# Kernel optimization log

Measured on AMD Instinct MI355X. Metric: run time of the kernel, lower is better.

Reference implementation:

```python
import jax, jax.numpy as jnp
import numpy as np
from jax import lax

B, T, D, H, L = 64, 512, 768, 256, 9


def _lstm_dir(x, Wih, Whh, b, reverse):
    # x: [B,T,in]; Wih: [4H,in]; Whh: [4H,H]; b: [4H] (b_ih + b_hh fused).
    # PyTorch LSTM gate order: i, f, g, o.
    Hh = Whh.shape[1]
    xg = jnp.einsum('bti,gi->btg', x, Wih) + b  # precompute input contribution [B,T,4H]

    def step(carry, xt):
        h, c = carry
        g = xt + h @ Whh.T
        i, f, gg, o = jnp.split(g, 4, axis=-1)
        c = jax.nn.sigmoid(f) * c + jax.nn.sigmoid(i) * jnp.tanh(gg)
        h = jax.nn.sigmoid(o) * jnp.tanh(c)
        return (h, c), h

    h0 = jnp.zeros((x.shape[0], Hh), x.dtype)
    _, hs = lax.scan(step, (h0, h0), jnp.swapaxes(xg, 0, 1), reverse=reverse)
    return jnp.swapaxes(hs, 0, 1)  # [B,T,H], time-aligned for both directions


def _bilstm_layer(x, Wih, Whh, b):
    fwd = _lstm_dir(x, Wih[0], Whh[0], b[0], False)
    bwd = _lstm_dir(x, Wih[1], Whh[1], b[1], True)
    return jnp.concatenate([fwd, bwd], axis=-1)  # [B,T,2H]


def _crf_nll(em, tags, start, end, trans):
    # em: [B,S,L] emissions, tags: [B,S], full (all-ones) mask; mean-reduced NLL.
    # Numerator: score of the gold path.
    num = start[tags[:, 0]] + end[tags[:, -1]]
    num = num + jnp.take_along_axis(em, tags[:, :, None], axis=2)[..., 0].sum(1)
    num = num + trans[tags[:, :-1], tags[:, 1:]].sum(1)
    # Denominator: forward algorithm (log partition) as a scan over time.

    def step(alpha, em_t):
        # alpha: [B,L]; em_t: [B,L]
        return jax.nn.logsumexp(alpha[:, :, None] + trans[None] + em_t[:, None, :], axis=1), None

    alpha, _ = lax.scan(step, start + em[:, 0], jnp.swapaxes(em[:, 1:], 0, 1))
    logZ = jax.nn.logsumexp(alpha + end, axis=1)
    return -(num - logZ).mean()


def setup_inputs() -> dict:
    key = jax.random.key(0)
    ks = jax.random.split(key, 13)
    s = 1.0 / np.sqrt(H)  # PyTorch LSTM/Linear-style uniform init
    u = lambda k, shape: jax.random.uniform(k, shape, jnp.float32, -s, s)
    return {
        'features': jax.random.normal(ks[0], (B, T, D), jnp.float32),
        'labels': jax.random.randint(ks[1], (B, T), 0, L),
        'mask': jnp.ones((B, T), jnp.bool_),
        'lstm0_Wih': u(ks[2], (2, 4 * H, D)),
        'lstm0_Whh': u(ks[3], (2, 4 * H, H)),
        'lstm0_b': u(ks[4], (2, 4 * H)),
        'lstm1_Wih': u(ks[5], (2, 4 * H, 2 * H)),
        'lstm1_Whh': u(ks[6], (2, 4 * H, H)),
        'lstm1_b': u(ks[7], (2, 4 * H)),
        'cls_W': u(ks[8], (L, 2 * H)),
        'cls_b': u(ks[9], (L,)),
        'crf_start': 0.1 * jax.random.normal(ks[10], (L,)),
        'crf_end': 0.1 * jax.random.normal(ks[11], (L,)),
        'crf_trans': 0.1 * jax.random.normal(ks[12], (L, L)),
    }


def reference(features, labels, mask, lstm0_Wih, lstm0_Whh, lstm0_b,
              lstm1_Wih, lstm1_Whh, lstm1_b, cls_W, cls_b,
              crf_start, crf_end, crf_trans):
    # Eval-mode dropout = identity. mask is all-ones, so pack_padded_sequence
    # degenerates to a plain full-length BiLSTM.
    h = _bilstm_layer(features, lstm0_Wih, lstm0_Whh, lstm0_b)
    h = _bilstm_layer(h, lstm1_Wih, lstm1_Whh, lstm1_b)
    logits = h @ cls_W.T + cls_b  # [B,T,L]
    # With a full mask the module's per-row masking loop keeps timesteps [1, T-1).
    loss = _crf_nll(logits[:, 1:-1], labels[:, 1:-1], crf_start, crf_end, crf_trans)
    return loss, logits
```

## Files before the change

kernel.cpp:

```cpp
#include <hip/hip_runtime.h>

typedef unsigned int uint32;
typedef unsigned short ushort16;
typedef __attribute__((ext_vector_type(8))) short short8;
typedef __attribute__((ext_vector_type(4))) float f32x4;

typedef __attribute__((address_space(1))) const unsigned char gbyte;
typedef __attribute__((address_space(3))) unsigned char lbyte;
#define GLDS16(g, l) __builtin_amdgcn_global_load_lds((gbyte*)(g), (lbyte*)(l), 16, 0, 0)

__device__ __forceinline__ float bf2f(ushort16 u) {
    return __uint_as_float(((uint32)u) << 16);
}
__device__ __forceinline__ float bflo(uint32 u) { return __uint_as_float(u << 16); }
__device__ __forceinline__ float bfhi(uint32 u) { return __uint_as_float(u & 0xffff0000u); }
__device__ __forceinline__ ushort16 f2bf(float f) {
    uint32 u = __float_as_uint(f);
    return (ushort16)((u + 0x7FFFu + ((u >> 16) & 1u)) >> 16);
}
__device__ __forceinline__ float sigm(float x) {
    return __builtin_amdgcn_rcpf(1.f + __expf(-x));
}
__device__ __forceinline__ float tanh_f(float x) {
    return 1.f - 2.f * __builtin_amdgcn_rcpf(__expf(2.f * x) + 1.f);
}
__device__ __forceinline__ int gated_zero(short8 dep) {
    int z; asm volatile("v_mov_b32 %0, 0" : "=v"(z) : "v"(dep)); return z;
}

__global__ __launch_bounds__(256) void k_cvt_bf16(const float* __restrict__ in,
                                                  ushort16* __restrict__ out, int n4) {
    int i = blockIdx.x * 256 + threadIdx.x;
    int stride = gridDim.x * 256;
    for (; i < n4; i += stride) {
        float4 v = ((const float4*)in)[i];
        ushort4 o;
        o.x = f2bf(v.x); o.y = f2bf(v.y); o.z = f2bf(v.z); o.w = f2bf(v.w);
        ((ushort4*)out)[i] = o;
    }
}

__global__ __launch_bounds__(256) void k_wfrag(const float* __restrict__ whh,
                                               ushort16* __restrict__ out) {
    int i = blockIdx.x * 256 + threadIdx.x;
    int j    = i & 7;
    int lane = (i >> 3) & 63;
    int kf   = (i >> 9) & 7;
    int nt   = (i >> 12) & 7;
    int w    = (i >> 15) & 7;
    int d    = (i >> 18) & 1;
    int g = nt >> 1, hh = nt & 1;
    int orow = g * 256 + w * 32 + hh * 16 + (lane & 15);
    int k = kf * 32 + (lane >> 4) * 8 + j;
    float v = whh[((size_t)d * 1024 + orow) * 256 + k];
    out[i] = f2bf(v);
}

__global__ __launch_bounds__(256) void k_gemm_xg(const ushort16* __restrict__ A,
                                                 const ushort16* __restrict__ Bt,
                                                 const float* __restrict__ bias,
                                                 ushort16* __restrict__ C,
                                                 int M, int N, int K, int tmaj) {
    __shared__ ushort16 As[128 * 32];
    __shared__ ushort16 Bs[128 * 32];
    const int tid = threadIdx.x;
    const int bm = blockIdx.x * 128, bn = blockIdx.y * 128;
    const int lane = tid & 63, wave = tid >> 6;
    const int wr = (wave >> 1) * 64, wc = (wave & 1) * 64;
    const int l15 = lane & 15, l4 = lane >> 4;
    f32x4 acc[4][4] = {};
    const int ar = tid >> 2;
    const int ac = (tid & 3) * 8;
    const size_t rowA  = (size_t)(bm + ar) * K;
    const size_t rowA2 = (size_t)(bm + ar + 64) * K;
    const size_t rowB  = (size_t)(bn + ar) * K;
    const size_t rowB2 = (size_t)(bn + ar + 64) * K;

    for (int k0 = 0; k0 < K; k0 += 32) {
        GLDS16(&A[rowA + k0 + ac],  &As[tid * 8]);
        GLDS16(&A[rowA2 + k0 + ac], &As[2048 + tid * 8]);
        GLDS16(&Bt[rowB + k0 + ac],  &Bs[tid * 8]);
        GLDS16(&Bt[rowB2 + k0 + ac], &Bs[2048 + tid * 8]);
        __builtin_amdgcn_sched_barrier(0);
        asm volatile("s_waitcnt vmcnt(0)" ::: "memory");
        __syncthreads();

        short8 af[4], bfv[4];
#pragma unroll
        for (int i = 0; i < 4; i++) {
            af[i]  = *(const short8*)&As[(wr + i * 16 + l15) * 32 + l4 * 8];
            bfv[i] = *(const short8*)&Bs[(wc + i * 16 + l15) * 32 + l4 * 8];
        }
#pragma unroll
        for (int mi = 0; mi < 4; mi++)
#pragma unroll
            for (int ni = 0; ni < 4; ni++)
                acc[mi][ni] = __builtin_amdgcn_mfma_f32_16x16x32_bf16(af[mi], bfv[ni],
                                                                     acc[mi][ni], 0, 0, 0);
        __syncthreads();
    }

#pragma unroll
    for (int mi = 0; mi < 4; mi++) {
#pragma unroll
        for (int ni = 0; ni < 4; ni++) {
            int col = bn + wc + ni * 16 + l15;
            float bv = bias[col];
            int dcol = col >> 10, g = (col >> 8) & 3;
            int wvv = (col >> 5) & 7, hh = (col >> 4) & 1, l15c = col & 15;
            int nt = g * 2 + hh;
#pragma unroll
            for (int r = 0; r < 4; r++) {
                int row = bm + wr + mi * 16 + l4 * 4 + r;
                int batch, tt;
                if (tmaj) { batch = row & 63; tt = row >> 6; }
                else      { batch = row >> 9; tt = row & 511; }
                int b4 = batch & 15;
                int lanec = ((b4 >> 2) << 4) | l15c;
                size_t idx2 = ((((size_t)((dcol << 2) | (batch >> 4)) * 512 + tt) * 8 + wvv) * 64
                               + lanec) * 32 + nt * 4 + (b4 & 3);
                C[idx2] = f2bf(acc[mi][ni][r] + bv);
            }
        }
    }
}

__global__ __launch_bounds__(512, 2) void k_lstm_scan5(const ushort16* __restrict__ xg2,
                                                       const ushort16* __restrict__ w2,
                                                       ushort16* __restrict__ hout) {
    extern __shared__ char smem[];
    ushort16* hf = (ushort16*)smem;
    ushort16* wl = (ushort16*)(smem + 16384);

    const int bg = blockIdx.x >> 1, d = blockIdx.x & 1;
    const int tid = threadIdx.x;
    const int wv = tid >> 6, lane = tid & 63;
    const int l15 = lane & 15, l4 = lane >> 4;
    const int swl = (lane ^ (lane >> 3)) * 8;
    const size_t dbase = (size_t)d * 262144;

    for (int q = tid; q < 1024; q += 512) ((uint4*)hf)[q] = make_uint4(0, 0, 0, 0);
    {
        const uint4* src = (const uint4*)(w2 + dbase);
        uint4* dst = (uint4*)wl;
        for (int q = tid; q < 8192; q += 512) {
            int sidx = q >> 7;
            int kp = (q >> 6) & 1;
            int off = q & 63;
            dst[q] = src[(sidx * 8 + 4 + kp) * 64 + off];
        }
    }
    const ushort16* wbase = w2 + dbase + (size_t)wv * 32768 + lane * 8;
    short8 wa[8][4];
#pragma unroll
    for (int nt = 0; nt < 8; ++nt)
#pragma unroll
        for (int kf = 0; kf < 4; ++kf)
            wa[nt][kf] = *(const short8*)&wbase[nt * 4096 + kf * 512];
    const ushort16* w6 = wbase + 6 * 512;
    __syncthreads();

    const int t0 = d ? 511 : 0;
    const int dstep = d ? -16384 : 16384;
    const int hstep = d ? -32768 : 32768;
    const ushort16* xp = xg2 + ((((size_t)(d * 4 + bg) * 512 + t0) * 8 + wv) * 64 + lane) * 32;
    ushort16* hp = hout + ((size_t)t0 * 32768 + (bg * 16 + l4 * 4) * 512 + d * 256 + wv * 32 + l15);

    int dsa[8];
#pragma unroll
    for (int hh = 0; hh < 2; ++hh)
#pragma unroll
        for (int r = 0; r < 4; ++r) {
            int lp = (hh * 2 + (l15 >> 3)) * 16 + l4 * 4 + r;
            int ch = lp ^ (lp >> 3);
            dsa[hh * 4 + r] = wv * 512 + ch * 8 + (l15 & 7);
        }

    uint4 xc0 = ((const uint4*)xp)[0];
    uint4 xc1 = ((const uint4*)xp)[1];
    uint4 xc2 = ((const uint4*)xp)[2];
    uint4 xc3 = ((const uint4*)xp)[3];
    float cst[8] = {0.f, 0.f, 0.f, 0.f, 0.f, 0.f, 0.f, 0.f};
    int cur = 0;

    for (int s = 0; s < 512; ++s) {
        xp += dstep;

        f32x4 acc[8];
        acc[0][0]=bflo(xc0.x); acc[0][1]=bfhi(xc0.x); acc[0][2]=bflo(xc0.y); acc[0][3]=bfhi(xc0.y);
        acc[1][0]=bflo(xc0.z); acc[1][1]=bfhi(xc0.z); acc[1][2]=bflo(xc0.w); acc[1][3]=bfhi(xc0.w);
        acc[2][0]=bflo(xc1.x); acc[2][1]=bfhi(xc1.x); acc[2][2]=bflo(xc1.y); acc[2][3]=bfhi(xc1.y);
        acc[3][0]=bflo(xc1.z); acc[3][1]=bfhi(xc1.z); acc[3][2]=bflo(xc1.w); acc[3][3]=bfhi(xc1.w);
        acc[4][0]=bflo(xc2.x); acc[4][1]=bfhi(xc2.x); acc[4][2]=bflo(xc2.y); acc[4][3]=bfhi(xc2.y);
        acc[5][0]=bflo(xc2.z); acc[5][1]=bfhi(xc2.z); acc[5][2]=bflo(xc2.w); acc[5][3]=bfhi(xc2.w);
        acc[6][0]=bflo(xc3.x); acc[6][1]=bfhi(xc3.x); acc[6][2]=bflo(xc3.y); acc[6][3]=bfhi(xc3.y);
        acc[7][0]=bflo(xc3.z); acc[7][1]=bfhi(xc3.z); acc[7][2]=bflo(xc3.w); acc[7][3]=bfhi(xc3.w);

        const ushort16* hcur = hf + cur * 4096;

        {
            short8 a4 = *(const short8*)&hcur[4 * 512 + swl];
#pragma unroll
            for (int nt = 0; nt < 8; ++nt) {
                short8 b = *(const short8*)&wl[((wv * 8 + nt) * 2 + 0) * 512 + lane * 8];
                acc[nt] = __builtin_amdgcn_mfma_f32_16x16x32_bf16(a4, b, acc[nt], 0, 0, 0);
            }
        }
        short8 a0 = *(const short8*)&hcur[0 * 512 + swl];
        int z0 = gated_zero(a0);
        short8 w6a[4];
#pragma unroll
        for (int nt = 0; nt < 4; ++nt) w6a[nt] = *(const short8*)&w6[nt * 4096 + z0];
#pragma unroll
        for (int nt = 0; nt < 8; ++nt)
            asm volatile("v_mfma_f32_16x16x32_bf16 %0, %1, %2, %0"
                         : "+v"(acc[nt]) : "v"(a0), "a"(wa[nt][0]));
        short8 a1 = *(const short8*)&hcur[1 * 512 + swl];
        int z1 = gated_zero(a1);
        short8 w6b[4];
#pragma unroll
        for (int nt = 0; nt < 4; ++nt) w6b[nt] = *(const short8*)&w6[(nt + 4) * 4096 + z1];
#pragma unroll
        for (int nt = 0; nt < 8; ++nt)
            asm volatile("v_mfma_f32_16x16x32_bf16 %0, %1, %2, %0"
                         : "+v"(acc[nt]) : "v"(a1), "a"(wa[nt][1]));
        short8 a2 = *(const short8*)&hcur[2 * 512 + swl];
        int z2 = gated_zero(a2);
        short8 w7a[4];
#pragma unroll
        for (int nt = 0; nt < 4; ++nt) w7a[nt] = *(const short8*)&w6[nt * 4096 + 512 + z2];
#pragma unroll
        for (int nt = 0; nt < 8; ++nt)
            asm volatile("v_mfma_f32_16x16x32_bf16 %0, %1, %2, %0"
                         : "+v"(acc[nt]) : "v"(a2), "a"(wa[nt][2]));
        short8 a6 = *(const short8*)&hcur[6 * 512 + swl];
#pragma unroll
        for (int nt = 0; nt < 4; ++nt)
            acc[nt] = __builtin_amdgcn_mfma_f32_16x16x32_bf16(a6, w6a[nt], acc[nt], 0, 0, 0);
        short8 a3 = *(const short8*)&hcur[3 * 512 + swl];
        int z3 = gated_zero(a3);
        short8 w7b[4];
#pragma unroll
        for (int nt = 0; nt < 4; ++nt) w7b[nt] = *(const short8*)&w6[(nt + 4) * 4096 + 512 + z3];
#pragma unroll
        for (int nt = 0; nt < 8; ++nt)
            asm volatile("v_mfma_f32_16x16x32_bf16 %0, %1, %2, %0"
                         : "+v"(acc[nt]) : "v"(a3), "a"(wa[nt][3]));
        uint4 xn0 = ((const uint4*)xp)[0];
        uint4 xn1 = ((const uint4*)xp)[1];
        uint4 xn2 = ((const uint4*)xp)[2];
        uint4 xn3 = ((const uint4*)xp)[3];
#pragma unroll
        for (int nt = 4; nt < 8; ++nt)
            acc[nt] = __builtin_amdgcn_mfma_f32_16x16x32_bf16(a6, w6b[nt - 4], acc[nt], 0, 0, 0);
        {
            short8 a5 = *(const short8*)&hcur[5 * 512 + swl];
#pragma unroll
            for (int nt = 0; nt < 8; ++nt) {
                short8 b = *(const short8*)&wl[((wv * 8 + nt) * 2 + 1) * 512 + lane * 8];
                acc[nt] = __builtin_amdgcn_mfma_f32_16x16x32_bf16(a5, b, acc[nt], 0, 0, 0);
            }
        }
        short8 a7 = *(const short8*)&hcur[7 * 512 + swl];
#pragma unroll
        for (int nt = 0; nt < 4; ++nt)
            acc[nt] = __builtin_amdgcn_mfma_f32_16x16x32_bf16(a7, w7a[nt], acc[nt], 0, 0, 0);
#pragma unroll
        for (int nt = 4; nt < 8; ++nt)
            acc[nt] = __builtin_amdgcn_mfma_f32_16x16x32_bf16(a7, w7b[nt - 4], acc[nt], 0, 0, 0);

        float hv[8];
#pragma unroll
        for (int hh = 0; hh < 2; ++hh)
#pragma unroll
            for (int r = 0; r < 4; ++r) {
                float ig = sigm(acc[0 + hh][r]);
                float fg = sigm(acc[2 + hh][r]);
                float gg = tanh_f(acc[4 + hh][r]);
                float og = sigm(acc[6 + hh][r]);
                float c = fg * cst[hh * 4 + r] + ig * gg;
                cst[hh * 4 + r] = c;
                hv[hh * 4 + r] = og * tanh_f(c);
            }
        uint32 p01, p23, p45, p67;
        asm volatile("v_cvt_pk_bf16_f32 %0, %1, %2" : "=v"(p01) : "v"(hv[0]), "v"(hv[1]));
        asm volatile("v_cvt_pk_bf16_f32 %0, %1, %2" : "=v"(p23) : "v"(hv[2]), "v"(hv[3]));
        asm volatile("v_cvt_pk_bf16_f32 %0, %1, %2" : "=v"(p45) : "v"(hv[4]), "v"(hv[5]));
        asm volatile("v_cvt_pk_bf16_f32 %0, %1, %2" : "=v"(p67) : "v"(hv[6]), "v"(hv[7]));
        ushort16 hb[8];
        hb[0] = (ushort16)p01; hb[1] = (ushort16)(p01 >> 16);
        hb[2] = (ushort16)p23; hb[3] = (ushort16)(p23 >> 16);
        hb[4] = (ushort16)p45; hb[5] = (ushort16)(p45 >> 16);
        hb[6] = (ushort16)p67; hb[7] = (ushort16)(p67 >> 16);

        ushort16* hnxt = hf + (cur ^ 1) * 4096;
#pragma unroll
        for (int hh = 0; hh < 2; ++hh)
#pragma unroll
            for (int r = 0; r < 4; ++r) {
                hnxt[dsa[hh * 4 + r]] = hb[hh * 4 + r];
                hp[r * 512 + hh * 16] = hb[hh * 4 + r];
            }
        hp += hstep;

        __builtin_amdgcn_sched_barrier(0);
        asm volatile("s_waitcnt lgkmcnt(0)" ::: "memory");
        __builtin_amdgcn_s_barrier();
        __builtin_amdgcn_sched_barrier(0);

        xc0 = xn0; xc1 = xn1; xc2 = xn2; xc3 = xn3;
        cur ^= 1;
    }
}

__global__ __launch_bounds__(256) void k_logits(const ushort16* __restrict__ h1,
                                                const float* __restrict__ Wc,
                                                const float* __restrict__ bc,
                                                float* __restrict__ out) {
    __shared__ ushort16 hs[16 * 512];
    __shared__ float wsm[9 * 512];
    __shared__ float bs[9];
    const int tid = threadIdx.x;
    const size_t row0 = (size_t)blockIdx.x * 16;
    const uint4* src = (const uint4*)(h1 + row0 * 512);
    uint4* dst = (uint4*)hs;
#pragma unroll
    for (int i = 0; i < 4; i++) dst[tid + i * 256] = src[tid + i * 256];
    for (int i = tid; i < 4608; i += 256) wsm[i] = Wc[i];
    if (tid < 9) bs[tid] = bc[tid];
    __syncthreads();
    if (tid < 144) {
        int r = tid / 9, l = tid - r * 9;
        float acc = bs[l];
        const ushort16* hr = &hs[r * 512];
        const float* wrow = &wsm[l * 512];
        for (int k = 0; k < 512; k++) acc += bf2f(hr[k]) * wrow[k];
        int rowidx = (int)row0 + r;
        int bb = rowidx & 63, tt = rowidx >> 6;
        out[((size_t)bb * 512 + tt) * 9 + l] = acc;
    }
}

__global__ __launch_bounds__(64) void k_crf(const float* __restrict__ logits,
                                            const int* __restrict__ labels,
                                            const float* __restrict__ start,
                                            const float* __restrict__ endv,
                                            const float* __restrict__ trans,
                                            float* __restrict__ perb) {
    const int b = blockIdx.x, lane = threadIdx.x;
    __shared__ float tr[81];
    __shared__ float emb[510 * 9];
    for (int i = lane; i < 81; i += 64) tr[i] = trans[i];
    const float* em = logits + (size_t)b * 512 * 9;
    for (int i = lane; i < 4590; i += 64) emb[i] = em[9 + i];
    __syncthreads();
    const int* lb = labels + (size_t)b * 512;

    float acc = 0.f;
    for (int s = lane; s < 510; s += 64) acc += emb[s * 9 + lb[s + 1]];
    for (int s = lane; s < 509; s += 64) acc += tr[lb[s + 1] * 9 + lb[s + 2]];
#pragma unroll
    for (int off = 32; off; off >>= 1) acc += __shfl_down(acc, off);

    const int j = (lane < 9) ? lane : 0;
    float alpha = start[j] + emb[j];
    for (int s = 1; s < 510; ++s) {
        float v[9];
        float m = -3.4e38f;
#pragma unroll
        for (int i = 0; i < 9; i++) {
            float ai = __shfl(alpha, i);
            float t = ai + tr[i * 9 + j];
            v[i] = t;
            m = fmaxf(m, t);
        }
        float sum = 0.f;
#pragma unroll
        for (int i = 0; i < 9; i++) sum += __expf(v[i] - m);
        alpha = m + __logf(sum) + emb[s * 9 + j];
    }
    float ae = alpha + endv[j];
    float mm = -3.4e38f;
#pragma unroll
    for (int i = 0; i < 9; i++) mm = fmaxf(mm, __shfl(ae, i));
    float ss = 0.f;
#pragma unroll
    for (int i = 0; i < 9; i++) ss += __expf(__shfl(ae, i) - mm);
    float logZ = mm + __logf(ss);
    if (lane == 0) {
        float num = acc + start[lb[1]] + endv[lb[510]];
        perb[b] = logZ - num;
    }
}

__global__ __launch_bounds__(64) void k_reduce(const float* __restrict__ perb,
                                               float* __restrict__ out) {
    float v = perb[threadIdx.x];
#pragma unroll
    for (int off = 32; off; off >>= 1) v += __shfl_down(v, off);
    if (threadIdx.x == 0) out[0] = v * (1.f / 64.f);
}

extern "C" void kernel_launch(void* const* d_in, const int* in_sizes, int n_in,
                              void* d_out, int out_size, void* d_ws, size_t ws_size,
                              hipStream_t stream) {
    const float* features = (const float*)d_in[0];
    const int*   labels   = (const int*)d_in[1];
    const float* w0ih = (const float*)d_in[3];
    const float* w0hh = (const float*)d_in[4];
    const float* b0   = (const float*)d_in[5];
    const float* w1ih = (const float*)d_in[6];
    const float* w1hh = (const float*)d_in[7];
    const float* b1   = (const float*)d_in[8];
    const float* clsW = (const float*)d_in[9];
    const float* clsb = (const float*)d_in[10];
    const float* cstart = (const float*)d_in[11];
    const float* cend   = (const float*)d_in[12];
    const float* ctrans = (const float*)d_in[13];

    char* ws = (char*)d_ws;
    ushort16* featbf = (ushort16*)(ws + 0);
    ushort16* h1buf  = (ushort16*)(ws + 0);
    ushort16* xg2    = (ushort16*)(ws + 50331648);
    ushort16* h0     = (ushort16*)(ws + 184549376);
    ushort16* wih0   = (ushort16*)(ws + 218103808);
    ushort16* wih1   = (ushort16*)(ws + 221249536);
    ushort16* w2_0   = (ushort16*)(ws + 223346688);
    ushort16* w2_1   = (ushort16*)(ws + 224395264);
    float*    perb   = (float*)(ws + 225443840);

    float* outF = (float*)d_out;
    float* logitsF = outF + 1;

    k_cvt_bf16<<<dim3(2048), dim3(256), 0, stream>>>(features, featbf, 25165824 / 4);
    k_cvt_bf16<<<dim3(512), dim3(256), 0, stream>>>(w0ih, wih0, 1572864 / 4);
    k_cvt_bf16<<<dim3(512), dim3(256), 0, stream>>>(w1ih, wih1, 1048576 / 4);
    k_wfrag<<<dim3(2048), dim3(256), 0, stream>>>(w0hh, w2_0);
    k_wfrag<<<dim3(2048), dim3(256), 0, stream>>>(w1hh, w2_1);

    k_gemm_xg<<<dim3(256, 16), dim3(256), 0, stream>>>(featbf, wih0, b0, xg2, 32768, 2048, 768, 0);
    k_lstm_scan5<<<dim3(8), dim3(512), 147456, stream>>>(xg2, w2_0, h0);
    k_gemm_xg<<<dim3(256, 16), dim3(256), 0, stream>>>(h0, wih1, b1, xg2, 32768, 2048, 512, 1);
    k_lstm_scan5<<<dim3(8), dim3(512), 147456, stream>>>(xg2, w2_1, h1buf);
    k_logits<<<dim3(2048), dim3(256), 0, stream>>>(h1buf, clsW, clsb, logitsF);
    k_crf<<<dim3(64), dim3(64), 0, stream>>>(logitsF, labels, cstart, cend, ctrans, perb);
    k_reduce<<<dim3(1), dim3(64), 0, stream>>>(perb, outF);
}
```

Baseline: 5.239 ms.

## Convert features to time-major bf16 and vectorize gate-precompute stores

The feature conversion kernel now writes bf16 in time-major order, so both GEMM launches use the time-major row mapping. Each 4-row accumulator group then lands in consecutive slots of the scan layout and is written with one 8-byte store instead of four scattered 2-byte stores. The scan kernel's gated-zero LDS offsets now depend on a cell-state value instead of the freshly loaded h fragments, which changes how the weight loads are ordered against the h loads. The transposed conversion adds a scattered write pattern in the feature conversion pass.

Result: faster. 4.692 ms (-10.4%).

```diff
diff --git a/kernel.cpp b/kernel.cpp
--- a/kernel.cpp
+++ b/kernel.cpp
@@ -24,7 +24,7 @@
 __device__ __forceinline__ float tanh_f(float x) {
     return 1.f - 2.f * __builtin_amdgcn_rcpf(__expf(2.f * x) + 1.f);
 }
-__device__ __forceinline__ int gated_zero(short8 dep) {
+__device__ __forceinline__ int gated_zero_f(float dep) {
     int z; asm volatile("v_mov_b32 %0, 0" : "=v"(z) : "v"(dep)); return z;
 }
 
@@ -37,6 +37,21 @@
         ushort4 o;
         o.x = f2bf(v.x); o.y = f2bf(v.y); o.z = f2bf(v.z); o.w = f2bf(v.w);
         ((ushort4*)out)[i] = o;
+    }
+}
+
+__global__ __launch_bounds__(256) void k_cvt_tmaj(const float* __restrict__ in,
+                                                  ushort16* __restrict__ out, int n4) {
+    int i = blockIdx.x * 256 + threadIdx.x;
+    int stride = gridDim.x * 256;
+    for (; i < n4; i += stride) {
+        float4 v = ((const float4*)in)[i];
+        int rem = i / 192;
+        int q = i - rem * 192;
+        int t = rem & 511, b = rem >> 9;
+        ushort4 o;
+        o.x = f2bf(v.x); o.y = f2bf(v.y); o.z = f2bf(v.z); o.w = f2bf(v.w);
+        ((ushort4*)out)[(t * 64 + b) * 192 + q] = o;
     }
 }
 
@@ -60,7 +75,7 @@
                                                  const ushort16* __restrict__ Bt,
                                                  const float* __restrict__ bias,
                                                  ushort16* __restrict__ C,
-                                                 int M, int N, int K, int tmaj) {
+                                                 int M, int N, int K) {
     __shared__ ushort16 As[128 * 32];
     __shared__ ushort16 Bs[128 * 32];
     const int tid = threadIdx.x;
@@ -109,18 +124,15 @@
             int dcol = col >> 10, g = (col >> 8) & 3;
             int wvv = (col >> 5) & 7, hh = (col >> 4) & 1, l15c = col & 15;
             int nt = g * 2 + hh;
-#pragma unroll
-            for (int r = 0; r < 4; r++) {
-                int row = bm + wr + mi * 16 + l4 * 4 + r;
-                int batch, tt;
-                if (tmaj) { batch = row & 63; tt = row >> 6; }
-                else      { batch = row >> 9; tt = row & 511; }
-                int b4 = batch & 15;
-                int lanec = ((b4 >> 2) << 4) | l15c;
-                size_t idx2 = ((((size_t)((dcol << 2) | (batch >> 4)) * 512 + tt) * 8 + wvv) * 64
-                               + lanec) * 32 + nt * 4 + (b4 & 3);
-                C[idx2] = f2bf(acc[mi][ni][r] + bv);
-            }
+            int row0 = bm + wr + mi * 16 + l4 * 4;
+            int batch0 = row0 & 63, tt = row0 >> 6;
+            int b4 = batch0 & 15;
+            int lanec = ((b4 >> 2) << 4) | l15c;
+            size_t base = ((((size_t)((dcol << 2) | (batch0 >> 4)) * 512 + tt) * 8 + wvv) * 64
+                           + lanec) * 32 + nt * 4;
+            uint32 lo = (uint32)f2bf(acc[mi][ni][0] + bv) | ((uint32)f2bf(acc[mi][ni][1] + bv) << 16);
+            uint32 hi = (uint32)f2bf(acc[mi][ni][2] + bv) | ((uint32)f2bf(acc[mi][ni][3] + bv) << 16);
+            *(uint2*)&C[base] = make_uint2(lo, hi);
         }
     }
 }
@@ -207,7 +219,7 @@
             }
         }
         short8 a0 = *(const short8*)&hcur[0 * 512 + swl];
-        int z0 = gated_zero(a0);
+        int z0 = gated_zero_f(cst[0]);
         short8 w6a[4];
 #pragma unroll
         for (int nt = 0; nt < 4; ++nt) w6a[nt] = *(const short8*)&w6[nt * 4096 + z0];
@@ -216,7 +228,7 @@
             asm volatile("v_mfma_f32_16x16x32_bf16 %0, %1, %2, %0"
                          : "+v"(acc[nt]) : "v"(a0), "a"(wa[nt][0]));
         short8 a1 = *(const short8*)&hcur[1 * 512 + swl];
-        int z1 = gated_zero(a1);
+        int z1 = gated_zero_f(cst[0]);
         short8 w6b[4];
 #pragma unroll
         for (int nt = 0; nt < 4; ++nt) w6b[nt] = *(const short8*)&w6[(nt + 4) * 4096 + z1];
@@ -225,7 +237,7 @@
             asm volatile("v_mfma_f32_16x16x32_bf16 %0, %1, %2, %0"
                          : "+v"(acc[nt]) : "v"(a1), "a"(wa[nt][1]));
         short8 a2 = *(const short8*)&hcur[2 * 512 + swl];
-        int z2 = gated_zero(a2);
+        int z2 = gated_zero_f(cst[0]);
         short8 w7a[4];
 #pragma unroll
         for (int nt = 0; nt < 4; ++nt) w7a[nt] = *(const short8*)&w6[nt * 4096 + 512 + z2];
@@ -238,7 +250,7 @@
         for (int nt = 0; nt < 4; ++nt)
             acc[nt] = __builtin_amdgcn_mfma_f32_16x16x32_bf16(a6, w6a[nt], acc[nt], 0, 0, 0);
         short8 a3 = *(const short8*)&hcur[3 * 512 + swl];
-        int z3 = gated_zero(a3);
+        int z3 = gated_zero_f(cst[0]);
         short8 w7b[4];
 #pragma unroll
         for (int nt = 0; nt < 4; ++nt) w7b[nt] = *(const short8*)&w6[(nt + 4) * 4096 + 512 + z3];
@@ -432,15 +444,15 @@
     float* outF = (float*)d_out;
     float* logitsF = outF + 1;
 
-    k_cvt_bf16<<<dim3(2048), dim3(256), 0, stream>>>(features, featbf, 25165824 / 4);
+    k_cvt_tmaj<<<dim3(2048), dim3(256), 0, stream>>>(features, featbf, 25165824 / 4);
     k_cvt_bf16<<<dim3(512), dim3(256), 0, stream>>>(w0ih, wih0, 1572864 / 4);
     k_cvt_bf16<<<dim3(512), dim3(256), 0, stream>>>(w1ih, wih1, 1048576 / 4);
     k_wfrag<<<dim3(2048), dim3(256), 0, stream>>>(w0hh, w2_0);
     k_wfrag<<<dim3(2048), dim3(256), 0, stream>>>(w1hh, w2_1);
 
-    k_gemm_xg<<<dim3(256, 16), dim3(256), 0, stream>>>(featbf, wih0, b0, xg2, 32768, 2048, 768, 0);
+    k_gemm_xg<<<dim3(256, 16), dim3(256), 0, stream>>>(featbf, wih0, b0, xg2, 32768, 2048, 768);
     k_lstm_scan5<<<dim3(8), dim3(512), 147456, stream>>>(xg2, w2_0, h0);
-    k_gemm_xg<<<dim3(256, 16), dim3(256), 0, stream>>>(h0, wih1, b1, xg2, 32768, 2048, 512, 1);
+    k_gemm_xg<<<dim3(256, 16), dim3(256), 0, stream>>>(h0, wih1, b1, xg2, 32768, 2048, 512);
     k_lstm_scan5<<<dim3(8), dim3(512), 147456, stream>>>(xg2, w2_1, h1buf);
     k_logits<<<dim3(2048), dim3(256), 0, stream>>>(h1buf, clsW, clsb, logitsF);
     k_crf<<<dim3(64), dim3(64), 0, stream>>>(logitsF, labels, cstart, cend, ctrans, perb);
```
